# Kernel tuning notes

Hardware: AMD Instinct MI355X
Metric: run time of the kernel (lower is better)

The kernel has to match this reference:

```python
import jax, jax.numpy as jnp
import numpy as np

# QuadFittingFromFlow: per-pixel quadratic least-squares fit from flow.
# The CUDA extension source is unavailable; this reference implements the
# standard per-pixel quadratic cost-surface fit it describes:
#  1. for each pixel p, bilinearly sample feat1 at p + flow + (ox,oy) for the
#     3x3 offset grid (ox,oy in {-1,0,1}) and compute the SSD matching cost
#     against feat0(p)  -> 9 cost samples c_k per pixel.
#  2. fit a 2D quadratic c(x,y) ~ a x^2 + b y^2 + c xy + d x + e y + f by
#     (softmin-)weighted least squares, solving the per-pixel 6x6 normal
#     equations. Output sol = the 6 quadratic coefficients per pixel (Y,X,6).
# The 3rd flow channel (validity/confidence) does not alter the LS solution
# (uniform per-pixel rescaling of weights) and is ignored, matching the
# module's docstring that only 2 displacement channels matter.

Y, X, L = 384, 512, 32
EPS = 1e-4  # Tikhonov regularization for the 6x6 solve

# fixed 3x3 offset grid and quadratic design matrix A (9 samples x 6 coeffs)
_oy, _ox = np.meshgrid(np.arange(-1, 2), np.arange(-1, 2), indexing='ij')
OFFS_X = jnp.asarray(_ox.reshape(-1), dtype=jnp.float32)  # (9,)
OFFS_Y = jnp.asarray(_oy.reshape(-1), dtype=jnp.float32)  # (9,)
_A = np.stack([_ox.reshape(-1) ** 2, _oy.reshape(-1) ** 2,
               _ox.reshape(-1) * _oy.reshape(-1),
               _ox.reshape(-1), _oy.reshape(-1),
               np.ones(9)], axis=1).astype(np.float32)
A_DESIGN = jnp.asarray(_A)  # (9, 6)


def _bilinear(feat, px, py):
    # feat: (Y,X,L); px,py: (Y,X,9) fractional sample coords -> (Y,X,9,L)
    Yd, Xd, _ = feat.shape
    x0f, y0f = jnp.floor(px), jnp.floor(py)
    wx = (px - x0f)[..., None]
    wy = (py - y0f)[..., None]
    x0 = jnp.clip(x0f.astype(jnp.int32), 0, Xd - 1)
    x1 = jnp.clip(x0 + 1, 0, Xd - 1)
    y0 = jnp.clip(y0f.astype(jnp.int32), 0, Yd - 1)
    y1 = jnp.clip(y0 + 1, 0, Yd - 1)
    f00 = feat[y0, x0]
    f01 = feat[y0, x1]
    f10 = feat[y1, x0]
    f11 = feat[y1, x1]
    return (f00 * (1 - wx) * (1 - wy) + f01 * wx * (1 - wy)
            + f10 * (1 - wx) * wy + f11 * wx * wy)


def _quadfit(t_feat0, t_feat1, t_flow):
    Yd, Xd, _ = t_feat0.shape
    u, v = t_flow[..., 0], t_flow[..., 1]  # displacement channels
    gy, gx = jnp.meshgrid(jnp.arange(Yd, dtype=jnp.float32),
                          jnp.arange(Xd, dtype=jnp.float32), indexing='ij')
    px = gx[..., None] + u[..., None] + OFFS_X  # (Y,X,9)
    py = gy[..., None] + v[..., None] + OFFS_Y
    samp = _bilinear(t_feat1, px, py)           # (Y,X,9,L)
    c = jnp.sum((t_feat0[:, :, None, :] - samp) ** 2, axis=-1)  # (Y,X,9)
    w = jax.nn.softmax(-c, axis=-1)             # robust per-pixel weights
    AtWA = jnp.einsum('ki,yxk,kj->yxij', A_DESIGN, w, A_DESIGN) \
        + EPS * jnp.eye(6, dtype=t_feat0.dtype)  # (Y,X,6,6)
    rhs = jnp.einsum('ki,yxk->yxi', A_DESIGN, w * c)  # (Y,X,6)
    sol = jnp.linalg.solve(AtWA, rhs[..., None])[..., 0]
    return sol  # (Y,X,6)


def setup_inputs() -> dict:
    key = jax.random.key(0)
    k0, k1, k2 = jax.random.split(key, 3)
    t_feat0 = jax.random.normal(k0, (Y, X, L), dtype=jnp.float32)
    t_feat1 = jax.random.normal(k1, (Y, X, L), dtype=jnp.float32)
    t_flow = jax.random.normal(k2, (Y, X, 3), dtype=jnp.float32) * 2.0
    return {"t_feat0": t_feat0, "t_feat1": t_feat1, "t_flow": t_flow}


def reference(t_feat0, t_feat1, t_flow):
    return _quadfit(t_feat0, t_feat1, t_flow)
```

## Files before the change

### kernel.cpp

```cpp
#include <hip/hip_runtime.h>
#include <math.h>

#define Ydim 384
#define Xdim 512
#define NPIX (Ydim * Xdim)
#define EPS 1e-4
#define PPB 128
#define NITER (PPB / 32)

__device__ __forceinline__ double fast_rcp64(double d) {
    double r = (double)__builtin_amdgcn_rcpf((float)d);
    r = r * (2.0 - d * r);
    r = r * (2.0 - d * r);
    return r;
}

__global__ __launch_bounds__(256, 2) void qf_fused_kernel(
    const float* __restrict__ feat0,
    const float* __restrict__ feat1,
    const float* __restrict__ flow,
    float* __restrict__ out)
{
    __shared__ float cost_lds[PPB * 9];

    const int t   = threadIdx.x;
    const int g   = t >> 3;
    const int sub = t & 7;

#pragma unroll 1
    for (int it = 0; it < NITER; ++it) {
        const int pb  = it * 32 + g;
        const int pix = blockIdx.x * PPB + pb;
        const int y = pix >> 9;
        const int x = pix & (Xdim - 1);

        const float u = flow[pix * 3 + 0];
        const float v = flow[pix * 3 + 1];
        const float4 f0 = *(const float4*)(feat0 + (size_t)pix * 32 + sub * 4);

        const float pxc = (float)x + u;
        const float pyc = (float)y + v;

        int   c0[3], c1[3], r0[3], r1[3];
        float wx[3], wy[3];
#pragma unroll
        for (int j = 0; j < 3; ++j) {
            float px = pxc + (float)(j - 1);
            float fx = floorf(px);
            wx[j] = px - fx;
            int xi = min(max((int)fx, 0), Xdim - 1);
            c0[j] = xi;
            c1[j] = min(xi + 1, Xdim - 1);
            float py = pyc + (float)(j - 1);
            float fy = floorf(py);
            wy[j] = py - fy;
            int yi = min(max((int)fy, 0), Ydim - 1);
            r0[j] = yi;
            r1[j] = min(yi + 1, Ydim - 1);
        }

        float cacc[9];
        const bool fast = (c1[0] == c0[1]) & (c1[1] == c0[2])
                        & (r1[0] == r0[1]) & (r1[1] == r0[2]);

        if (fast) {
            const int cols[4] = {c0[0], c0[1], c0[2], c1[2]};
            const int rows[4] = {r0[0], r0[1], r0[2], r1[2]};
            float4 F[4][4];
#pragma unroll
            for (int r = 0; r < 4; ++r) {
                const float* rb = feat1 + ((size_t)rows[r] * Xdim) * 32 + sub * 4;
#pragma unroll
                for (int c = 0; c < 4; ++c)
                    F[r][c] = *(const float4*)(rb + (size_t)cols[c] * 32);
            }
#pragma unroll
            for (int r = 0; r < 4; ++r)
#pragma unroll
                for (int c = 0; c < 4; ++c)
                    asm volatile("" : "+v"(F[r][c].x), "+v"(F[r][c].y),
                                      "+v"(F[r][c].z), "+v"(F[r][c].w));
#pragma unroll
            for (int i = 0; i < 3; ++i) {
                float wyv = wy[i], omwy = 1.f - wyv;
#pragma unroll
                for (int j = 0; j < 3; ++j) {
                    float wxv = wx[j], omwx = 1.f - wxv;
                    float w00 = omwx * omwy, w01 = wxv * omwy;
                    float w10 = omwx * wyv,  w11 = wxv * wyv;
                    float4 a = F[i][j], b = F[i][j + 1], c = F[i + 1][j], d = F[i + 1][j + 1];
                    float dx = f0.x - (a.x * w00 + b.x * w01 + c.x * w10 + d.x * w11);
                    float dy = f0.y - (a.y * w00 + b.y * w01 + c.y * w10 + d.y * w11);
                    float dz = f0.z - (a.z * w00 + b.z * w01 + c.z * w10 + d.z * w11);
                    float dw = f0.w - (a.w * w00 + b.w * w01 + c.w * w10 + d.w * w11);
                    cacc[i * 3 + j] = dx * dx + dy * dy + dz * dz + dw * dw;
                }
            }
        } else {
#pragma unroll
            for (int i = 0; i < 3; ++i) {
                float wyv = wy[i], omwy = 1.f - wyv;
                int rb0 = r0[i] * (Xdim * 32);
                int rb1 = r1[i] * (Xdim * 32);
#pragma unroll
                for (int j = 0; j < 3; ++j) {
                    const float4 f00 = *(const float4*)(feat1 + rb0 + c0[j] * 32 + sub * 4);
                    const float4 f01 = *(const float4*)(feat1 + rb0 + c1[j] * 32 + sub * 4);
                    const float4 f10 = *(const float4*)(feat1 + rb1 + c0[j] * 32 + sub * 4);
                    const float4 f11 = *(const float4*)(feat1 + rb1 + c1[j] * 32 + sub * 4);
                    float wxv = wx[j], omwx = 1.f - wxv;
                    float w00 = omwx * omwy, w01 = wxv * omwy;
                    float w10 = omwx * wyv,  w11 = wxv * wyv;
                    float dx = f0.x - (f00.x * w00 + f01.x * w01 + f10.x * w10 + f11.x * w11);
                    float dy = f0.y - (f00.y * w00 + f01.y * w01 + f10.y * w10 + f11.y * w11);
                    float dz = f0.z - (f00.z * w00 + f01.z * w01 + f10.z * w10 + f11.z * w11);
                    float dw = f0.w - (f00.w * w00 + f01.w * w01 + f10.w * w10 + f11.w * w11);
                    cacc[i * 3 + j] = dx * dx + dy * dy + dz * dz + dw * dw;
                }
            }
        }

#pragma unroll
        for (int m = 1; m <= 4; m <<= 1) {
#pragma unroll
            for (int k = 0; k < 9; ++k)
                cacc[k] += __shfl_xor(cacc[k], m);
        }
        if (sub == 0) {
#pragma unroll
            for (int k = 0; k < 9; ++k)
                cost_lds[pb * 9 + k] = cacc[k];
        }
    }
    __syncthreads();

    const int lane = t & 63;
    if (lane < 32) {
        const int pb = (t >> 6) * 32 + lane;

        float c[9];
#pragma unroll
        for (int k = 0; k < 9; ++k) c[k] = cost_lds[pb * 9 + k];

        float cmin = c[0];
#pragma unroll
        for (int k = 1; k < 9; ++k) cmin = fminf(cmin, c[k]);

        float e[9], sumf = 0.f;
#pragma unroll
        for (int k = 0; k < 9; ++k) {
            e[k] = expf(cmin - c[k]);
            sumf += e[k];
        }
        float invs = 1.f / sumf;

        float w[9], q[9];
#pragma unroll
        for (int k = 0; k < 9; ++k) {
            w[k] = e[k] * invs;
            q[k] = w[k] * c[k];
        }

        float sc0 = w[0] + w[3] + w[6], sc2 = w[2] + w[5] + w[8];
        float sr0 = w[0] + w[1] + w[2], sr2 = w[6] + w[7] + w[8];
        float S10 = sc2 - sc0, S20 = sc2 + sc0;
        float S01 = sr2 - sr0, S02 = sr2 + sr0;
        float S11 = (w[0] + w[8]) - (w[2] + w[6]);
        float S21 = (w[6] + w[8]) - (w[0] + w[2]);
        float S12 = (w[2] + w[8]) - (w[0] + w[6]);
        float S22 = w[0] + w[2] + w[6] + w[8];
        float S00 = sr0 + w[3] + w[4] + w[5] + sr2;

        float qc0 = q[0] + q[3] + q[6], qc2 = q[2] + q[5] + q[8];
        float qr0 = q[0] + q[1] + q[2], qr2 = q[6] + q[7] + q[8];
        float T10 = qc2 - qc0, T20 = qc2 + qc0;
        float T01 = qr2 - qr0, T02 = qr2 + qr0;
        float T11 = (q[0] + q[8]) - (q[2] + q[6]);
        float T00 = qr0 + q[3] + q[4] + q[5] + qr2;

        double M[6][6], rhs[6], ip[6];
        M[0][0] = (double)S20 + EPS; M[0][1] = S22; M[0][2] = S11; M[0][3] = S10; M[0][4] = S21; M[0][5] = S20;
        M[1][1] = (double)S02 + EPS; M[1][2] = S11; M[1][3] = S12; M[1][4] = S01; M[1][5] = S02;
        M[2][2] = (double)S22 + EPS; M[2][3] = S21; M[2][4] = S12; M[2][5] = S11;
        M[3][3] = (double)S20 + EPS; M[3][4] = S11; M[3][5] = S10;
        M[4][4] = (double)S02 + EPS; M[4][5] = S01;
        M[5][5] = (double)S00 + EPS;
        rhs[0] = T20; rhs[1] = T02; rhs[2] = T11; rhs[3] = T10; rhs[4] = T01; rhs[5] = T00;

#pragma unroll
        for (int p = 0; p < 6; ++p) {
            ip[p] = fast_rcp64(M[p][p]);
#pragma unroll
            for (int r = p + 1; r < 6; ++r) {
                double f = M[p][r] * ip[p];
#pragma unroll
                for (int cc = r; cc < 6; ++cc)
                    M[r][cc] -= f * M[p][cc];
                rhs[r] -= f * rhs[p];
            }
        }
        double sol[6];
#pragma unroll
        for (int p = 5; p >= 0; --p) {
            double s2 = rhs[p];
#pragma unroll
            for (int cc = p + 1; cc < 6; ++cc) s2 -= M[p][cc] * sol[cc];
            sol[p] = s2 * ip[p];
        }

        const int opix = blockIdx.x * PPB + pb;
#pragma unroll
        for (int i = 0; i < 6; ++i) out[(size_t)opix * 6 + i] = (float)sol[i];
    }
}

extern "C" void kernel_launch(void* const* d_in, const int* in_sizes, int n_in,
                              void* d_out, int out_size, void* d_ws, size_t ws_size,
                              hipStream_t stream) {
    const float* feat0 = (const float*)d_in[0];
    const float* feat1 = (const float*)d_in[1];
    const float* flow  = (const float*)d_in[2];
    float* out = (float*)d_out;

    qf_fused_kernel<<<dim3(NPIX / PPB), dim3(256), 0, stream>>>(feat0, feat1, flow, out);
}
```

Before: 107.0 us.

## Split fused kernel into cost kernel and separate solve kernel via workspace

Splits the fused kernel in two. The first kernel computes the nine SSD costs per pixel with high occupancy and streams feature rows to cut register pressure, then writes the costs to a planar workspace. The second kernel runs softmax and the 6x6 double solve with all lanes active, where before only half of each wave did this work. This trades an extra launch and about 7 MB of workspace traffic for better occupancy and lane utilization; the fused kernel remains as a fallback when no workspace is provided.

Result: slower. 231.9 us (+116.7%).

```diff
diff --git a/kernel.cpp b/kernel.cpp
--- a/kernel.cpp
+++ b/kernel.cpp
@@ -13,6 +13,207 @@
     r = r * (2.0 - d * r);
     r = r * (2.0 - d * r);
     return r;
+}
+
+__global__ __launch_bounds__(256, 8) void qf_cost_kernel(
+    const float* __restrict__ feat0,
+    const float* __restrict__ feat1,
+    const float* __restrict__ flow,
+    float* __restrict__ cost)
+{
+    __shared__ float cost_lds[32 * 9];
+
+    const int t   = threadIdx.x;
+    const int g   = t >> 3;
+    const int sub = t & 7;
+    const int pix = blockIdx.x * 32 + g;
+    const int y = pix >> 9;
+    const int x = pix & (Xdim - 1);
+
+    const float u = flow[pix * 3 + 0];
+    const float v = flow[pix * 3 + 1];
+    const float4 f0 = *(const float4*)(feat0 + (size_t)pix * 32 + sub * 4);
+
+    const float pxc = (float)x + u;
+    const float pyc = (float)y + v;
+
+    int   c0[3], c1[3], r0[3], r1[3];
+    float wx[3], wy[3];
+#pragma unroll
+    for (int j = 0; j < 3; ++j) {
+        float px = pxc + (float)(j - 1);
+        float fx = floorf(px);
+        wx[j] = px - fx;
+        int xi = min(max((int)fx, 0), Xdim - 1);
+        c0[j] = xi;
+        c1[j] = min(xi + 1, Xdim - 1);
+        float py = pyc + (float)(j - 1);
+        float fy = floorf(py);
+        wy[j] = py - fy;
+        int yi = min(max((int)fy, 0), Ydim - 1);
+        r0[j] = yi;
+        r1[j] = min(yi + 1, Ydim - 1);
+    }
+
+    float cacc[9];
+    const bool fast = (c1[0] == c0[1]) & (c1[1] == c0[2])
+                    & (r1[0] == r0[1]) & (r1[1] == r0[2]);
+
+    if (fast) {
+        const int cols[4] = {c0[0], c0[1], c0[2], c1[2]};
+        const int rows[4] = {r0[0], r0[1], r0[2], r1[2]};
+        float4 Fp[4], Fc[4];
+        {
+            const float* rb = feat1 + ((size_t)rows[0] * Xdim) * 32 + sub * 4;
+#pragma unroll
+            for (int c = 0; c < 4; ++c)
+                Fp[c] = *(const float4*)(rb + (size_t)cols[c] * 32);
+        }
+#pragma unroll
+        for (int i = 0; i < 3; ++i) {
+            const float* rb = feat1 + ((size_t)rows[i + 1] * Xdim) * 32 + sub * 4;
+#pragma unroll
+            for (int c = 0; c < 4; ++c)
+                Fc[c] = *(const float4*)(rb + (size_t)cols[c] * 32);
+            float wyv = wy[i], omwy = 1.f - wyv;
+#pragma unroll
+            for (int j = 0; j < 3; ++j) {
+                float wxv = wx[j], omwx = 1.f - wxv;
+                float w00 = omwx * omwy, w01 = wxv * omwy;
+                float w10 = omwx * wyv,  w11 = wxv * wyv;
+                float4 a = Fp[j], b = Fp[j + 1], c = Fc[j], d = Fc[j + 1];
+                float dx = f0.x - (a.x * w00 + b.x * w01 + c.x * w10 + d.x * w11);
+                float dy = f0.y - (a.y * w00 + b.y * w01 + c.y * w10 + d.y * w11);
+                float dz = f0.z - (a.z * w00 + b.z * w01 + c.z * w10 + d.z * w11);
+                float dw = f0.w - (a.w * w00 + b.w * w01 + c.w * w10 + d.w * w11);
+                cacc[i * 3 + j] = dx * dx + dy * dy + dz * dz + dw * dw;
+            }
+#pragma unroll
+            for (int c = 0; c < 4; ++c) Fp[c] = Fc[c];
+        }
+    } else {
+#pragma unroll
+        for (int i = 0; i < 3; ++i) {
+            float wyv = wy[i], omwy = 1.f - wyv;
+            int rb0 = r0[i] * (Xdim * 32);
+            int rb1 = r1[i] * (Xdim * 32);
+#pragma unroll
+            for (int j = 0; j < 3; ++j) {
+                const float4 f00 = *(const float4*)(feat1 + rb0 + c0[j] * 32 + sub * 4);
+                const float4 f01 = *(const float4*)(feat1 + rb0 + c1[j] * 32 + sub * 4);
+                const float4 f10 = *(const float4*)(feat1 + rb1 + c0[j] * 32 + sub * 4);
+                const float4 f11 = *(const float4*)(feat1 + rb1 + c1[j] * 32 + sub * 4);
+                float wxv = wx[j], omwx = 1.f - wxv;
+                float w00 = omwx * omwy, w01 = wxv * omwy;
+                float w10 = omwx * wyv,  w11 = wxv * wyv;
+                float dx = f0.x - (f00.x * w00 + f01.x * w01 + f10.x * w10 + f11.x * w11);
+                float dy = f0.y - (f00.y * w00 + f01.y * w01 + f10.y * w10 + f11.y * w11);
+                float dz = f0.z - (f00.z * w00 + f01.z * w01 + f10.z * w10 + f11.z * w11);
+                float dw = f0.w - (f00.w * w00 + f01.w * w01 + f10.w * w10 + f11.w * w11);
+                cacc[i * 3 + j] = dx * dx + dy * dy + dz * dz + dw * dw;
+            }
+        }
+    }
+
+#pragma unroll
+    for (int m = 1; m <= 4; m <<= 1) {
+#pragma unroll
+        for (int k = 0; k < 9; ++k)
+            cacc[k] += __shfl_xor(cacc[k], m);
+    }
+    if (sub == 0) {
+#pragma unroll
+        for (int k = 0; k < 9; ++k)
+            cost_lds[g * 9 + k] = cacc[k];
+    }
+    __syncthreads();
+
+    {
+        const int k = t >> 5, p = t & 31;
+        cost[(size_t)k * NPIX + blockIdx.x * 32 + p] = cost_lds[p * 9 + k];
+        if (t < 32)
+            cost[(size_t)8 * NPIX + blockIdx.x * 32 + t] = cost_lds[t * 9 + 8];
+    }
+}
+
+__global__ __launch_bounds__(256, 4) void qf_solve_kernel(
+    const float* __restrict__ cost,
+    float* __restrict__ out)
+{
+    const int pix = blockIdx.x * 256 + threadIdx.x;
+
+    float c[9];
+#pragma unroll
+    for (int k = 0; k < 9; ++k) c[k] = cost[(size_t)k * NPIX + pix];
+
+    float cmin = c[0];
+#pragma unroll
+    for (int k = 1; k < 9; ++k) cmin = fminf(cmin, c[k]);
+
+    float e[9], sumf = 0.f;
+#pragma unroll
+    for (int k = 0; k < 9; ++k) {
+        e[k] = expf(cmin - c[k]);
+        sumf += e[k];
+    }
+    float invs = 1.f / sumf;
+
+    float w[9], q[9];
+#pragma unroll
+    for (int k = 0; k < 9; ++k) {
+        w[k] = e[k] * invs;
+        q[k] = w[k] * c[k];
+    }
+
+    float sc0 = w[0] + w[3] + w[6], sc2 = w[2] + w[5] + w[8];
+    float sr0 = w[0] + w[1] + w[2], sr2 = w[6] + w[7] + w[8];
+    float S10 = sc2 - sc0, S20 = sc2 + sc0;
+    float S01 = sr2 - sr0, S02 = sr2 + sr0;
+    float S11 = (w[0] + w[8]) - (w[2] + w[6]);
+    float S21 = (w[6] + w[8]) - (w[0] + w[2]);
+    float S12 = (w[2] + w[8]) - (w[0] + w[6]);
+    float S22 = w[0] + w[2] + w[6] + w[8];
+    float S00 = sr0 + w[3] + w[4] + w[5] + sr2;
+
+    float qc0 = q[0] + q[3] + q[6], qc2 = q[2] + q[5] + q[8];
+    float qr0 = q[0] + q[1] + q[2], qr2 = q[6] + q[7] + q[8];
+    float T10 = qc2 - qc0, T20 = qc2 + qc0;
+    float T01 = qr2 - qr0, T02 = qr2 + qr0;
+    float T11 = (q[0] + q[8]) - (q[2] + q[6]);
+    float T00 = qr0 + q[3] + q[4] + q[5] + qr2;
+
+    double M[6][6], rhs[6], ip[6];
+    M[0][0] = (double)S20 + EPS; M[0][1] = S22; M[0][2] = S11; M[0][3] = S10; M[0][4] = S21; M[0][5] = S20;
+    M[1][1] = (double)S02 + EPS; M[1][2] = S11; M[1][3] = S12; M[1][4] = S01; M[1][5] = S02;
+    M[2][2] = (double)S22 + EPS; M[2][3] = S21; M[2][4] = S12; M[2][5] = S11;
+    M[3][3] = (double)S20 + EPS; M[3][4] = S11; M[3][5] = S10;
+    M[4][4] = (double)S02 + EPS; M[4][5] = S01;
+    M[5][5] = (double)S00 + EPS;
+    rhs[0] = T20; rhs[1] = T02; rhs[2] = T11; rhs[3] = T10; rhs[4] = T01; rhs[5] = T00;
+
+#pragma unroll
+    for (int p = 0; p < 6; ++p) {
+        ip[p] = fast_rcp64(M[p][p]);
+#pragma unroll
+        for (int r = p + 1; r < 6; ++r) {
+            double f = M[p][r] * ip[p];
+#pragma unroll
+            for (int cc = r; cc < 6; ++cc)
+                M[r][cc] -= f * M[p][cc];
+            rhs[r] -= f * rhs[p];
+        }
+    }
+    double sol[6];
+#pragma unroll
+    for (int p = 5; p >= 0; --p) {
+        double s2 = rhs[p];
+#pragma unroll
+        for (int cc = p + 1; cc < 6; ++cc) s2 -= M[p][cc] * sol[cc];
+        sol[p] = s2 * ip[p];
+    }
+
+#pragma unroll
+    for (int i = 0; i < 6; ++i) out[(size_t)pix * 6 + i] = (float)sol[i];
 }
 
 __global__ __launch_bounds__(256, 2) void qf_fused_kernel(
@@ -222,5 +423,12 @@
     const float* flow  = (const float*)d_in[2];
     float* out = (float*)d_out;
 
-    qf_fused_kernel<<<dim3(NPIX / PPB), dim3(256), 0, stream>>>(feat0, feat1, flow, out);
+    const size_t need = (size_t)9 * NPIX * sizeof(float);
+    if (d_ws != nullptr && ws_size >= need) {
+        float* cost = (float*)d_ws;
+        qf_cost_kernel<<<dim3(NPIX / 32), dim3(256), 0, stream>>>(feat0, feat1, flow, cost);
+        qf_solve_kernel<<<dim3(NPIX / 256), dim3(256), 0, stream>>>(cost, out);
+    } else {
+        qf_fused_kernel<<<dim3(NPIX / PPB), dim3(256), 0, stream>>>(feat0, feat1, flow, out);
+    }
 }
```
